# Optimization experiments

Measured on AMD Instinct MI355X. Metric: run time of the kernel, lower is better.

Reference implementation:

```python
import jax, jax.numpy as jnp
import numpy as np

N_TOK, BATCH, D, MEM, H, W = 196, 64, 256, 2048, 16, 16


def setup_inputs() -> dict:
    key = jax.random.key(0)
    ks = jax.random.split(key, 9)
    w_scale = 1.0 / np.sqrt(D)  # ~ Linear default init scale
    return {
        "input_tokens": jax.random.normal(ks[0], (N_TOK, BATCH, D), jnp.float32),
        "ch_memory": jax.random.normal(ks[1], (MEM, D), jnp.float32) * 0.1,
        "ch_wq": jax.random.normal(ks[2], (D, D), jnp.float32) * w_scale,
        "ch_wk": jax.random.normal(ks[3], (D, D), jnp.float32) * w_scale,
        "ch_wv": jax.random.normal(ks[4], (D, D), jnp.float32) * w_scale,
        "sp_memory": jax.random.normal(ks[5], (MEM, H, W), jnp.float32) * 0.1,
        "sp_wq": jax.random.normal(ks[6], (D, D), jnp.float32) * w_scale,
        "sp_wk": jax.random.normal(ks[7], (D, D), jnp.float32) * w_scale,
        "sp_wv": jax.random.normal(ks[8], (D, D), jnp.float32) * w_scale,
    }


def reference(input_tokens, ch_memory, ch_wq, ch_wk, ch_wv,
              sp_memory, sp_wq, sp_wk, sp_wv):
    n_tok, batch, d = input_tokens.shape
    hw = d  # spatial branch requires feature_dim == H*W
    x = input_tokens.reshape(n_tok * batch, d)  # [NB, D]

    # ---- Channel memory branch: dot-product softmax read ----
    q = x @ ch_wq.T                       # [NB, D]
    k = ch_memory @ ch_wk.T               # [M, D]
    v = ch_memory @ ch_wv.T               # [M, D]
    scores = (q @ k.T) * (1.0 / jnp.sqrt(jnp.float32(d)))  # [NB, M]
    att_c = jax.nn.softmax(scores, axis=-1)
    out_c = att_c @ v                     # [NB, D]

    # ---- Spatial memory branch: SSIM-score softmax read ----
    mem_flat = sp_memory.reshape(sp_memory.shape[0], hw)  # [M, HW]
    qf = x @ sp_wq.T                      # [NB, HW]
    kf = mem_flat @ sp_wk.T               # [M, HW]
    vf = mem_flat @ sp_wv.T               # [M, HW]

    q_mean = jnp.mean(qf, axis=1, keepdims=True)          # [NB, 1]
    k_mean = jnp.mean(kf, axis=1, keepdims=True)          # [M, 1]
    q_var = jnp.var(qf, axis=1, ddof=1, keepdims=True)    # unbiased, like torch.var
    k_var = jnp.var(kf, axis=1, ddof=1, keepdims=True)
    cov = ((qf - q_mean) @ (kf - k_mean).T) / jnp.float32(hw - 1)  # [NB, M]

    c1, c2 = 0.01, 0.03
    mean_prod = q_mean @ k_mean.T                          # [NB, M]
    numerator = (2.0 * mean_prod + c1) * (2.0 * cov + c2)
    denominator = (q_mean ** 2 + (k_mean.T) ** 2 + c1) * (q_var + k_var.T + c2)
    ssim = numerator / (denominator + 1e-8)                # [NB, M]

    att_s = jax.nn.softmax(ssim, axis=-1)
    out_s = att_s @ vf                     # [NB, HW] == [NB, D]

    return (out_c + out_s).reshape(n_tok, batch, d)
```

## Files before the change

kernel.cpp:

```cpp
#include <hip/hip_runtime.h>

#define NBQ 12544
#define DM  256
#define MM  2048

typedef __attribute__((ext_vector_type(8)))  __bf16 bf16x8;
typedef __attribute__((ext_vector_type(4)))  float  floatx4;

__device__ __forceinline__ ushort f2bf(float x) {
    unsigned u = __float_as_uint(x);
    u += 0x7fffu + ((u >> 16) & 1u);
    return (ushort)(u >> 16);
}
__device__ __forceinline__ float bf2f(ushort h) {
    return __uint_as_float(((unsigned)h) << 16);
}

__global__ __launch_bounds__(256) void gemm_proj_all(
    const float* __restrict__ x,      const float* __restrict__ ch_mem,
    const float* __restrict__ ch_wq,  const float* __restrict__ ch_wk,
    const float* __restrict__ ch_wv,  const float* __restrict__ sp_mem,
    const float* __restrict__ sp_wq,  const float* __restrict__ sp_wk,
    const float* __restrict__ sp_wv,
    ushort* __restrict__ Qb,  ushort* __restrict__ QFb,
    ushort* __restrict__ Kb,  ushort* __restrict__ KFb,
    ushort* __restrict__ Vtb, ushort* __restrict__ VFtb)
{
    __shared__ ushort As[64][72];
    __shared__ ushort Ws[64][72];

    int bid = blockIdx.x;
    const float* A; const float* W; ushort* C; int nrows, trans;
    if (bid < 1568) {
        if (bid < 784) { A = x; W = ch_wq; C = Qb; }
        else           { A = x; W = sp_wq; C = QFb; bid -= 784; }
        nrows = NBQ; trans = 0;
    } else if (bid < 1824) {
        if (bid < 1696) { A = ch_mem; W = ch_wk; C = Kb;  bid -= 1568; }
        else            { A = sp_mem; W = sp_wk; C = KFb; bid -= 1696; }
        nrows = MM; trans = 0;
    } else {
        if (bid < 1952) { A = ch_mem; W = ch_wv; C = Vtb;  bid -= 1824; }
        else            { A = sp_mem; W = sp_wv; C = VFtb; bid -= 1952; }
        nrows = MM; trans = 1;
    }
    const int r0 = (bid >> 2) * 64;
    const int c0 = (bid & 3) * 64;

    const int tid  = threadIdx.x;
    const int wv   = tid >> 6;
    const int lane = tid & 63;
    const int quad = lane >> 4;
    const int l16  = lane & 15;
    const int rw = (wv & 1) * 32;
    const int cw = (wv >> 1) * 32;

    floatx4 acc[2][2];
    #pragma unroll
    for (int i = 0; i < 2; ++i)
        #pragma unroll
        for (int j = 0; j < 2; ++j)
            acc[i][j] = (floatx4){0.f, 0.f, 0.f, 0.f};

    for (int d0 = 0; d0 < 256; d0 += 64) {
        __syncthreads();
        #pragma unroll
        for (int it = 0; it < 4; ++it) {
            int idx = tid + it * 256;
            int r = idx >> 4, c4 = (idx & 15) * 4;
            float4 a4 = *(const float4*)(A + (size_t)(r0 + r) * 256 + d0 + c4);
            float4 w4 = *(const float4*)(W + (size_t)(c0 + r) * 256 + d0 + c4);
            ushort4 ab, wb;
            ab.x = f2bf(a4.x); ab.y = f2bf(a4.y); ab.z = f2bf(a4.z); ab.w = f2bf(a4.w);
            wb.x = f2bf(w4.x); wb.y = f2bf(w4.y); wb.z = f2bf(w4.z); wb.w = f2bf(w4.w);
            *(ushort4*)&As[r][c4] = ab;
            *(ushort4*)&Ws[r][c4] = wb;
        }
        __syncthreads();
        #pragma unroll
        for (int kk = 0; kk < 64; kk += 32) {
            bf16x8 aA0 = *(const bf16x8*)&As[rw + l16][kk + quad * 8];
            bf16x8 aA1 = *(const bf16x8*)&As[rw + 16 + l16][kk + quad * 8];
            bf16x8 bW0 = *(const bf16x8*)&Ws[cw + l16][kk + quad * 8];
            bf16x8 bW1 = *(const bf16x8*)&Ws[cw + 16 + l16][kk + quad * 8];
            acc[0][0] = __builtin_amdgcn_mfma_f32_16x16x32_bf16(aA0, bW0, acc[0][0], 0, 0, 0);
            acc[0][1] = __builtin_amdgcn_mfma_f32_16x16x32_bf16(aA0, bW1, acc[0][1], 0, 0, 0);
            acc[1][0] = __builtin_amdgcn_mfma_f32_16x16x32_bf16(aA1, bW0, acc[1][0], 0, 0, 0);
            acc[1][1] = __builtin_amdgcn_mfma_f32_16x16x32_bf16(aA1, bW1, acc[1][1], 0, 0, 0);
        }
    }

    if (!trans) {
        #pragma unroll
        for (int ag = 0; ag < 2; ++ag)
            #pragma unroll
            for (int cg = 0; cg < 2; ++cg)
                #pragma unroll
                for (int i = 0; i < 4; ++i)
                    C[(size_t)(r0 + rw + ag * 16 + quad * 4 + i) * 256
                      + c0 + cw + cg * 16 + l16] = f2bf(acc[ag][cg][i]);
    } else {
        __syncthreads();
        #pragma unroll
        for (int ag = 0; ag < 2; ++ag)
            #pragma unroll
            for (int cg = 0; cg < 2; ++cg)
                #pragma unroll
                for (int i = 0; i < 4; ++i)
                    Ws[cw + cg * 16 + l16][rw + ag * 16 + quad * 4 + i] = f2bf(acc[ag][cg][i]);
        __syncthreads();
        const int col = tid >> 2;
        const int seg = (tid & 3) * 16;
        #pragma unroll
        for (int j = 0; j < 2; ++j)
            *(uint4*)(C + (size_t)(c0 + col) * nrows + r0 + seg + j * 8) =
                *(const uint4*)&Ws[col][seg + j * 8];
    }
}

__global__ __launch_bounds__(256) void row_stats_all(
    const ushort* __restrict__ QFb, const ushort* __restrict__ KFb,
    float* __restrict__ qm, float* __restrict__ qv,
    float* __restrict__ km, float* __restrict__ kv)
{
    const int rt   = blockIdx.x * 4 + (threadIdx.x >> 6);
    const int lane = threadIdx.x & 63;
    const ushort* X; float* mean; float* var; int row;
    if (rt < NBQ) { X = QFb; mean = qm; var = qv; row = rt; }
    else          { X = KFb; mean = km; var = kv; row = rt - NBQ; }
    ushort4 u = *(const ushort4*)(X + (size_t)row * 256 + lane * 4);
    float a = bf2f(u.x), b = bf2f(u.y), c = bf2f(u.z), d = bf2f(u.w);
    float s  = a + b + c + d;
    float ss = a * a + b * b + c * c + d * d;
    #pragma unroll
    for (int off = 32; off > 0; off >>= 1) {
        s  += __shfl_down(s, off);
        ss += __shfl_down(ss, off);
    }
    if (lane == 0) {
        float m = s * (1.f / 256.f);
        mean[row] = m;
        var[row]  = (ss - 256.f * m * m) * (1.f / 255.f);
    }
}

__global__ __launch_bounds__(256, 3) void fused_attn_32q(
    const ushort* __restrict__ Qb,  const ushort* __restrict__ QFb,
    const ushort* __restrict__ Kb,  const ushort* __restrict__ KFb,
    const ushort* __restrict__ Vtb, const ushort* __restrict__ VFtb,
    const float* __restrict__ qm_, const float* __restrict__ qv_,
    const float* __restrict__ km_, const float* __restrict__ kv_,
    float* __restrict__ out)
{
    __shared__ ushort K_lds[32][264];
    __shared__ ushort Vt_lds[256][40];
    __shared__ ushort P_lds[32][40];
    __shared__ float  denbuf[2][32];

    const int tid  = threadIdx.x;
    const int wv   = tid >> 6;
    const int lane = tid & 63;
    const int quad = lane >> 4;
    const int l16  = lane & 15;
    const int qh   = wv & 1;
    const int kh   = wv >> 1;

    const bool spatial = (blockIdx.x >= 392);
    const int q0 = (spatial ? (int)blockIdx.x - 392 : (int)blockIdx.x) * 32;
    const ushort* Qp = spatial ? QFb  : Qb;
    const ushort* Kp = spatial ? KFb  : Kb;
    const ushort* Vp = spatial ? VFtb : Vtb;

    bf16x8 aQ[8];
    {
        const ushort* qp = Qp + (size_t)(q0 + qh * 16 + l16) * DM + quad * 8;
        #pragma unroll
        for (int s = 0; s < 8; ++s) aQ[s] = *(const bf16x8*)(qp + s * 32);
    }
    float qmr[4], qvr[4];
    if (spatial) {
        #pragma unroll
        for (int r = 0; r < 4; ++r) {
            int row = q0 + qh * 16 + quad * 4 + r;
            qmr[r] = qm_[row]; qvr[r] = qv_[row];
        }
    }

    floatx4 accO[2][4];
    #pragma unroll
    for (int a = 0; a < 2; ++a)
        #pragma unroll
        for (int b = 0; b < 4; ++b)
            accO[a][b] = (floatx4){0.f, 0.f, 0.f, 0.f};
    float den_r[4] = {0.f, 0.f, 0.f, 0.f};

    for (int kt = 0; kt < MM; kt += 32) {
        __syncthreads();
        #pragma unroll
        for (int it = 0; it < 4; ++it) {
            int idx = tid + it * 256;
            int r = idx >> 5, c8 = (idx & 31) * 8;
            *(uint4*)&K_lds[r][c8] = *(const uint4*)(Kp + (size_t)(kt + r) * DM + c8);
        }
        #pragma unroll
        for (int it = 0; it < 4; ++it) {
            int idx = tid + it * 256;
            int d = idx >> 2, kc = idx & 3;
            *(uint4*)&Vt_lds[d][kc * 8] = *(const uint4*)(Vp + (size_t)d * MM + kt + kc * 8);
        }
        __syncthreads();

        floatx4 S = (floatx4){0.f, 0.f, 0.f, 0.f};
        #pragma unroll
        for (int s = 0; s < 8; ++s) {
            bf16x8 bK = *(const bf16x8*)&K_lds[kh * 16 + l16][s * 32 + quad * 8];
            S = __builtin_amdgcn_mfma_f32_16x16x32_bf16(aQ[s], bK, S, 0, 0, 0);
        }
        {
            int kcol = kt + kh * 16 + l16;
            float kmv = 0.f, kvv = 0.f;
            if (spatial) { kmv = km_[kcol]; kvv = kv_[kcol]; }
            #pragma unroll
            for (int r = 0; r < 4; ++r) {
                float p;
                if (!spatial) {
                    p = __expf(S[r] * 0.0625f);
                } else {
                    float mp  = qmr[r] * kmv;
                    float cov = (S[r] - 256.f * mp) * (1.f / 255.f);
                    float num = (2.f * mp + 0.01f) * (2.f * cov + 0.03f);
                    float den = (qmr[r] * qmr[r] + kmv * kmv + 0.01f) * (qvr[r] + kvv + 0.03f);
                    p = __expf(num / (den + 1e-8f));
                }
                P_lds[qh * 16 + quad * 4 + r][kh * 16 + l16] = f2bf(p);
                den_r[r] += p;
            }
        }
        __syncthreads();

        bf16x8 aP0 = *(const bf16x8*)&P_lds[l16][quad * 8];
        bf16x8 aP1 = *(const bf16x8*)&P_lds[16 + l16][quad * 8];
        #pragma unroll
        for (int ds = 0; ds < 4; ++ds) {
            bf16x8 bV = *(const bf16x8*)&Vt_lds[wv * 64 + ds * 16 + l16][quad * 8];
            accO[0][ds] = __builtin_amdgcn_mfma_f32_16x16x32_bf16(aP0, bV, accO[0][ds], 0, 0, 0);
            accO[1][ds] = __builtin_amdgcn_mfma_f32_16x16x32_bf16(aP1, bV, accO[1][ds], 0, 0, 0);
        }
    }

    #pragma unroll
    for (int r = 0; r < 4; ++r)
        #pragma unroll
        for (int m = 1; m < 16; m <<= 1)
            den_r[r] += __shfl_xor(den_r[r], m, 64);
    if (l16 == 0) {
        #pragma unroll
        for (int r = 0; r < 4; ++r)
            denbuf[kh][qh * 16 + quad * 4 + r] = den_r[r];
    }
    __syncthreads();

    #pragma unroll
    for (int qt = 0; qt < 2; ++qt) {
        #pragma unroll
        for (int r = 0; r < 4; ++r) {
            int rloc = qt * 16 + quad * 4 + r;
            float rden = 1.f / (denbuf[0][rloc] + denbuf[1][rloc]);
            #pragma unroll
            for (int ds = 0; ds < 4; ++ds)
                atomicAdd(out + (size_t)(q0 + rloc) * DM + wv * 64 + ds * 16 + l16,
                          accO[qt][ds][r] * rden);
        }
    }
}

extern "C" void kernel_launch(void* const* d_in, const int* in_sizes, int n_in,
                              void* d_out, int out_size, void* d_ws, size_t ws_size,
                              hipStream_t stream)
{
    const float* x      = (const float*)d_in[0];
    const float* ch_mem = (const float*)d_in[1];
    const float* ch_wq  = (const float*)d_in[2];
    const float* ch_wk  = (const float*)d_in[3];
    const float* ch_wv  = (const float*)d_in[4];
    const float* sp_mem = (const float*)d_in[5];
    const float* sp_wq  = (const float*)d_in[6];
    const float* sp_wk  = (const float*)d_in[7];
    const float* sp_wv  = (const float*)d_in[8];
    float* out = (float*)d_out;

    ushort* Qb   = (ushort*)d_ws;
    ushort* QFb  = Qb   + (size_t)NBQ * DM;
    ushort* Kb   = QFb  + (size_t)NBQ * DM;
    ushort* KFb  = Kb   + (size_t)MM * DM;
    ushort* Vtb  = KFb  + (size_t)MM * DM;
    ushort* VFtb = Vtb  + (size_t)MM * DM;
    float*  qm   = (float*)(VFtb + (size_t)MM * DM);
    float*  qv   = qm + NBQ;
    float*  km   = qv + NBQ;
    float*  kv   = km + MM;

    hipMemsetAsync(out, 0, (size_t)NBQ * DM * sizeof(float), stream);

    dim3 blk(256);
    gemm_proj_all<<<dim3(2080), blk, 0, stream>>>(
        x, ch_mem, ch_wq, ch_wk, ch_wv, sp_mem, sp_wq, sp_wk, sp_wv,
        Qb, QFb, Kb, KFb, Vtb, VFtb);
    row_stats_all<<<dim3((NBQ + MM) / 4), blk, 0, stream>>>(QFb, KFb, qm, qv, km, kv);
    fused_attn_32q<<<dim3(784), blk, 0, stream>>>(
        Qb, QFb, Kb, KFb, Vtb, VFtb, qm, qv, km, kv, out);
}
```

Baseline: 302.7 us.

## Register-prefetch next K/V tile and repack V tile LDS layout

Loads for the next K and V tile are issued into registers right after the LDS store barrier. They overlap with the current tile's QK and PV MFMA work instead of stalling at the start of each iteration. The V^T tile is repacked from a [256][40] layout into [128][72], folding two d-halves into one row, and P_lds padding shrinks. The cost is 32 extra VGPRs for prefetch buffers, which may pressure the 3-block occupancy target.

```diff
diff --git a/kernel.cpp b/kernel.cpp
--- a/kernel.cpp
+++ b/kernel.cpp
@@ -153,8 +153,8 @@
     float* __restrict__ out)
 {
     __shared__ ushort K_lds[32][264];
-    __shared__ ushort Vt_lds[256][40];
-    __shared__ ushort P_lds[32][40];
+    __shared__ ushort VV_lds[128][72];
+    __shared__ ushort P_lds[32][36];
     __shared__ float  denbuf[2][32];
 
     const int tid  = threadIdx.x;
@@ -171,6 +171,21 @@
     const ushort* Kp = spatial ? KFb  : Kb;
     const ushort* Vp = spatial ? VFtb : Vtb;
 
+    int kr[4], kc8[4], vrow[4], vcol[4];
+    size_t vgoff[4];
+    #pragma unroll
+    for (int it = 0; it < 4; ++it) {
+        int idx = tid + it * 256;
+        kr[it]  = idx >> 5;
+        kc8[it] = (idx & 31) * 8;
+        int r  = idx >> 3;
+        int c  = idx & 7;
+        int dhi = c >> 2, kc = c & 3;
+        vrow[it]  = r;
+        vcol[it]  = dhi * 32 + kc * 8;
+        vgoff[it] = (size_t)(r + dhi * 128) * MM + kc * 8;
+    }
+
     bf16x8 aQ[8];
     {
         const ushort* qp = Qp + (size_t)(q0 + qh * 16 + l16) * DM + quad * 8;
@@ -194,21 +209,29 @@
             accO[a][b] = (floatx4){0.f, 0.f, 0.f, 0.f};
     float den_r[4] = {0.f, 0.f, 0.f, 0.f};
 
+    uint4 kreg[4], vreg[4];
+    #pragma unroll
+    for (int it = 0; it < 4; ++it) {
+        kreg[it] = *(const uint4*)(Kp + (size_t)kr[it] * DM + kc8[it]);
+        vreg[it] = *(const uint4*)(Vp + vgoff[it]);
+    }
+
     for (int kt = 0; kt < MM; kt += 32) {
         __syncthreads();
         #pragma unroll
         for (int it = 0; it < 4; ++it) {
-            int idx = tid + it * 256;
-            int r = idx >> 5, c8 = (idx & 31) * 8;
-            *(uint4*)&K_lds[r][c8] = *(const uint4*)(Kp + (size_t)(kt + r) * DM + c8);
-        }
-        #pragma unroll
-        for (int it = 0; it < 4; ++it) {
-            int idx = tid + it * 256;
-            int d = idx >> 2, kc = idx & 3;
-            *(uint4*)&Vt_lds[d][kc * 8] = *(const uint4*)(Vp + (size_t)d * MM + kt + kc * 8);
-        }
-        __syncthreads();
+            *(uint4*)&K_lds[kr[it]][kc8[it]]   = kreg[it];
+            *(uint4*)&VV_lds[vrow[it]][vcol[it]] = vreg[it];
+        }
+        __syncthreads();
+
+        if (kt + 32 < MM) {
+            #pragma unroll
+            for (int it = 0; it < 4; ++it) {
+                kreg[it] = *(const uint4*)(Kp + (size_t)(kt + 32 + kr[it]) * DM + kc8[it]);
+                vreg[it] = *(const uint4*)(Vp + vgoff[it] + kt + 32);
+            }
+        }
 
         floatx4 S = (floatx4){0.f, 0.f, 0.f, 0.f};
         #pragma unroll
@@ -242,7 +265,8 @@
         bf16x8 aP1 = *(const bf16x8*)&P_lds[16 + l16][quad * 8];
         #pragma unroll
         for (int ds = 0; ds < 4; ++ds) {
-            bf16x8 bV = *(const bf16x8*)&Vt_lds[wv * 64 + ds * 16 + l16][quad * 8];
+            int d = wv * 64 + ds * 16 + l16;
+            bf16x8 bV = *(const bf16x8*)&VV_lds[d & 127][(d >> 7) * 32 + quad * 8];
             accO[0][ds] = __builtin_amdgcn_mfma_f32_16x16x32_bf16(aP0, bV, accO[0][ds], 0, 0, 0);
             accO[1][ds] = __builtin_amdgcn_mfma_f32_16x16x32_bf16(aP1, bV, accO[1][ds], 0, 0, 0);
         }
```

Result: slower. 773.2 us (+155.5%).
